# Kernel optimization log

Measured on AMD Instinct MI355X. Metric: run time of the kernel, lower is better.

Reference implementation:

```python
import jax, jax.numpy as jnp
import numpy as np

CLASS_NUM = 31
KERNEL_NUM = 5
KERNEL_MUL = 2.0


def setup_inputs() -> dict:
    key = jax.random.key(0)
    k1, k2, k3, k4 = jax.random.split(key, 4)
    B, D = 4096, 256
    source = jax.random.normal(k1, (B, D), dtype=jnp.float32)
    target = jax.random.normal(k2, (B, D), dtype=jnp.float32)
    s_label = jax.random.randint(k3, (B,), 0, CLASS_NUM, dtype=jnp.int64)
    t_label = jax.random.uniform(k4, (B, CLASS_NUM), dtype=jnp.float32)
    return {"source": source, "target": target, "s_label": s_label, "t_label": t_label}


def _cal_weight(s_label, t_label):
    # Source: one-hot, column-normalized (empty classes -> divide by 100)
    s_onehot = jax.nn.one_hot(s_label, CLASS_NUM, dtype=jnp.float32)
    s_cnt = jnp.sum(s_onehot, axis=0)
    s_vec = s_onehot / jnp.where(s_cnt == 0, 100.0, s_cnt)
    # Target: soft probs, column-normalized (detached in original)
    t_prob = jax.lax.stop_gradient(t_label)
    t_cnt = jnp.sum(t_prob, axis=0)
    t_vec = t_prob / jnp.where(t_cnt == 0, 100.0, t_cnt)
    # Classes present in BOTH source labels and target argmax predictions
    t_arg = jnp.argmax(t_prob, axis=1)
    t_present = jnp.sum(jax.nn.one_hot(t_arg, CLASS_NUM, dtype=jnp.float32), axis=0) > 0
    mask = ((s_cnt > 0) & t_present).astype(jnp.float32)
    n_idx = jnp.maximum(jnp.sum(mask), 1.0)
    s_vec = s_vec * mask
    t_vec = t_vec * mask
    w_ss = (s_vec @ s_vec.T) / n_idx
    w_tt = (t_vec @ t_vec.T) / n_idx
    w_st = (s_vec @ t_vec.T) / n_idx
    return w_ss, w_tt, w_st


def reference(source, target, s_label, t_label):
    B = source.shape[0]
    w_ss, w_tt, w_st = _cal_weight(s_label, t_label)

    # Multi-bandwidth RBF kernel over concatenated samples
    total = jnp.concatenate([source, target], axis=0)  # [2B, D]
    sq = jnp.sum(total * total, axis=1)
    l2 = jnp.maximum(sq[:, None] + sq[None, :] - 2.0 * (total @ total.T), 0.0)  # [2B, 2B]

    n = 2 * B
    bw = jnp.sum(jax.lax.stop_gradient(l2)) / float(max(n * n - n, 1))
    bw = jnp.maximum(bw, 1e-6) / (KERNEL_MUL ** (KERNEL_NUM // 2))
    kernels = jnp.zeros_like(l2)
    for i in range(KERNEL_NUM):
        kernels = kernels + jnp.exp(-l2 / jnp.maximum(bw * KERNEL_MUL ** i, 1e-6))

    ss = kernels[:B, :B]
    tt = kernels[B:, B:]
    st = kernels[:B, B:]
    loss = jnp.sum(w_ss * ss + w_tt * tt - 2.0 * w_st * st)
    return loss
```

## Files before the change

### kernel.cpp

```cpp
#include <hip/hip_runtime.h>
#include <cstddef>


#define B 4096
#define D 256
#define C 31
#define N2 8192
#define NTILE 64
#define NBLK (NTILE * (NTILE + 1) / 2)

typedef __attribute__((ext_vector_type(8))) short bf16x8;
typedef __attribute__((ext_vector_type(4))) float f32x4;

struct WS {
  float inv_n_idx;
  float inv_d4;
  float pSumsq[256];
  unsigned pTpres[128];
  alignas(16) float pMsum[256 * 256];
  alignas(16) int pScnt[128 * 32];
  alignas(16) float pTcnt[128 * 32];
  float sq[N2];
  int slab[N2];
  float sdv[N2];
  alignas(16) unsigned char Thi8[(size_t)N2 * D];
  alignas(16) unsigned short vhi[(size_t)N2 * 32];
  alignas(16) double part[NBLK];
};

static __device__ __forceinline__ unsigned short f2bf(float f) {
  unsigned int u = __float_as_uint(f);
  return (unsigned short)((u + 0x7fffu + ((u >> 16) & 1u)) >> 16);
}
static __device__ __forceinline__ float bf2f(unsigned short s) {
  return __uint_as_float(((unsigned int)s) << 16);
}
static __device__ __forceinline__ float exp2_hw(float x) {
  float r;
  asm("v_exp_f32 %0, %1" : "=v"(r) : "v"(x));
  return r;
}

#define GLD16(gsrc, ldst)                                                     \
  __builtin_amdgcn_global_load_lds(                                           \
      (const __attribute__((address_space(1))) void*)(gsrc),                  \
      (__attribute__((address_space(3))) void*)(ldst), 16, 0, 0)

__global__ __launch_bounds__(256) void kPrep(const float* __restrict__ src,
                                             const float* __restrict__ tgt,
                                             const int* __restrict__ s_label,
                                             const float* __restrict__ t_label,
                                             WS* __restrict__ ws) {
  int tid = threadIdx.x, w = tid >> 6, lane = tid & 63;
  int blk = blockIdx.x;
  int r0 = blk * 32;
  bool is_src = (r0 < B);
  __shared__ float rsq[32];
  __shared__ float colp[4][256];
  __shared__ int ls[32];
  __shared__ float lt[8][32];
  __shared__ int lpres[32];
  if (tid < 32) { ls[tid] = 0; lpres[tid] = 0; }

  const float* basep =
      is_src ? src + (size_t)r0 * D : tgt + (size_t)(r0 - B) * D;

  float4 xv[8];
#pragma unroll
  for (int i = 0; i < 8; ++i)
    xv[i] = *(const float4*)(basep + (size_t)(w * 8 + i) * D + lane * 4);

  float ca0 = 0.f, ca1 = 0.f, ca2 = 0.f, ca3 = 0.f;
  int sc = lane >> 4, gl = (lane >> 1) & 7, hf = lane & 1;
#pragma unroll
  for (int i = 0; i < 8; ++i) {
    int rr = w * 8 + i;
    int p = r0 + rr;
    float4 x = xv[i];
    unsigned int pk = __builtin_amdgcn_cvt_pk_fp8_f32(x.x, x.y, 0, false);
    pk = __builtin_amdgcn_cvt_pk_fp8_f32(x.z, x.w, pk, true);
    int gp = (gl + p + (p >> 1)) & 7;
    *(unsigned int*)(&ws->Thi8[(size_t)p * D + sc * 64 + gp * 8 + hf * 4]) = pk;
    ca0 += x.x; ca1 += x.y; ca2 += x.z; ca3 += x.w;
    float s = x.x * x.x + x.y * x.y + x.z * x.z + x.w * x.w;
#pragma unroll
    for (int off = 32; off; off >>= 1) s += __shfl_down(s, off, 64);
    if (lane == 0) rsq[rr] = s;
  }
  colp[w][lane * 4 + 0] = ca0;
  colp[w][lane * 4 + 1] = ca1;
  colp[w][lane * 4 + 2] = ca2;
  colp[w][lane * 4 + 3] = ca3;

  if (!is_src) {
    int g = tid >> 5, c = tid & 31;
    float s = 0.f;
    if (c < C) {
#pragma unroll
      for (int k = 0; k < 4; ++k)
        s += t_label[(size_t)(r0 - B + g * 4 + k) * C + c];
    }
    lt[g][c] = s;
    int rr = tid >> 3, j = tid & 7;
    float best = -1e30f;
    int barg = 0;
    for (int c2 = j; c2 < C; c2 += 8) {
      float x = t_label[(size_t)(r0 - B + rr) * C + c2];
      if (x > best) { best = x; barg = c2; }
    }
#pragma unroll
    for (int m = 1; m < 8; m <<= 1) {
      float ob = __shfl_xor(best, m, 64);
      int oa = __shfl_xor(barg, m, 64);
      if (ob > best || (ob == best && oa < barg)) { best = ob; barg = oa; }
    }
    if (j == 0) lpres[barg] = 1;
  }
  __syncthreads();

  if (tid < 32) {
    int p = r0 + tid;
    ws->sq[p] = rsq[tid];
    if (is_src) {
      int lb = s_label[p];
      ws->slab[p] = lb;
      atomicAdd(&ls[lb], 1);
    } else {
      ws->slab[p] = 0;
    }
  }
  if (tid < 64) {
    float ss = (tid < 32) ? rsq[tid] : 0.f;
#pragma unroll
    for (int off = 32; off; off >>= 1) ss += __shfl_down(ss, off, 64);
    if (tid == 0) ws->pSumsq[blk] = ss;
  }
  ws->pMsum[blk * 256 + tid] =
      colp[0][tid] + colp[1][tid] + colp[2][tid] + colp[3][tid];
  __syncthreads();
  if (is_src) {
    if (tid < 32) ws->pScnt[blk * 32 + tid] = ls[tid];
  } else {
    if (tid < 32) {
      float s = 0.f;
#pragma unroll
      for (int g = 0; g < 8; ++g) s += lt[g][tid];
      ws->pTcnt[(blk - 128) * 32 + tid] = s;
    }
    if (tid < 64) {
      int bit = (tid < 32) ? lpres[tid] : 0;
      unsigned long long bal = __ballot(bit != 0);
      if (tid == 0) ws->pTpres[blk - 128] = (unsigned)bal;
    }
  }
}

__global__ __launch_bounds__(256) void kFin(const float* __restrict__ t_label,
                                            WS* __restrict__ ws) {
  int tid = threadIdx.x, w = tid >> 6, lane = tid & 63;
  __shared__ float sdiv[32], tdiv[32];
  __shared__ int rs[8][32];
  __shared__ float rt[8][32];
  __shared__ unsigned pm[2];
  __shared__ double dm[4], dsq[4];

  {
    int g = tid >> 5, c = tid & 31;
    int cs = 0;
    float ts = 0.f;
#pragma unroll
    for (int k = 0; k < 16; ++k) {
      cs += ws->pScnt[(g * 16 + k) * 32 + c];
      ts += ws->pTcnt[(g * 16 + k) * 32 + c];
    }
    rs[g][c] = cs;
    rt[g][c] = ts;
  }
  if (tid < 128) {
    unsigned m = ws->pTpres[tid];
#pragma unroll
    for (int off = 32; off; off >>= 1) m |= __shfl_down(m, off, 64);
    if ((tid & 63) == 0) pm[tid >> 6] = m;
  }
  __syncthreads();

  if (tid < 64) {
    int m = 0;
    if (tid < 32) {
      int cnt = 0;
      float t = 0.f;
#pragma unroll
      for (int g = 0; g < 8; ++g) { cnt += rs[g][tid]; t += rt[g][tid]; }
      unsigned pres = pm[0] | pm[1];
      m = (tid < C) && (cnt > 0) && ((pres >> tid) & 1u);
      sdiv[tid] = m ? 1.f / (float)cnt : 0.f;
      tdiv[tid] = m ? 1.f / ((t == 0.f) ? 100.f : t) : 0.f;
    }
    unsigned long long bal = __ballot(m);
    if (tid == 0 && blockIdx.x == 0)
      ws->inv_n_idx = 1.f / fmaxf((float)__popcll(bal), 1.f);
  }

  if (blockIdx.x == 0) {
    double m = 0.0;
    for (int b2 = 0; b2 < 256; ++b2) m += (double)ws->pMsum[b2 * 256 + tid];
    double msq = m * m;
    double ssq = (double)ws->pSumsq[tid];
#pragma unroll
    for (int off = 32; off; off >>= 1) {
      msq += __shfl_down(msq, off, 64);
      ssq += __shfl_down(ssq, off, 64);
    }
    if (lane == 0) { dm[w] = msq; dsq[w] = ssq; }
    __syncthreads();
    if (tid == 0) {
      double MSQ = dm[0] + dm[1] + dm[2] + dm[3];
      double S = dsq[0] + dsq[1] + dsq[2] + dsq[3];
      double n = (double)N2;
      double sum_l2 = 2.0 * n * S - 2.0 * MSQ;
      double bw = sum_l2 / (n * n - n);
      bw = fmax(bw, 1e-6) * 0.25;
      ws->inv_d4 = (float)(1.0 / fmax(bw * 16.0, 1e-6));
    }
  }
  __syncthreads();

  int p = blockIdx.x * 256 + tid;
  if (p < B) {
    ws->sdv[p] = sdiv[ws->slab[p]];
  } else {
    ws->sdv[p] = 0.f;
    const float* r = t_label + (size_t)(p - B) * C;
    float vrow[32];
#pragma unroll
    for (int c = 0; c < 32; ++c) vrow[c] = (c < C) ? -r[c] * tdiv[c] : 0.f;
#pragma unroll
    for (int k = 0; k < 8; ++k) {
      ushort4 vh;
      vh.x = f2bf(vrow[k * 4 + 0]);
      vh.y = f2bf(vrow[k * 4 + 1]);
      vh.z = f2bf(vrow[k * 4 + 2]);
      vh.w = f2bf(vrow[k * 4 + 3]);
      *(ushort4*)(&ws->vhi[(size_t)p * 32 + k * 4]) = vh;
    }
  }
}

template <int KIND, bool DIAG>
static __device__ __forceinline__ float epi_ss_st(
    const f32x4 (&acc)[4][4], float ci2, const float* tSq, const int* tSlab,
    const float* tSdv, const unsigned short* Vsw, int p0, int q0, int wr,
    int wc, int mrow, int quad) {
  float k2 = 2.f * ci2;
  float cq[4], sdq[4];
  int lq[4];
#pragma unroll
  for (int tj = 0; tj < 4; ++tj) {
    int iq = 128 + wc + tj * 16 + mrow;
    cq[tj] = -ci2 * tSq[iq];
    if (KIND == 0) {
      lq[tj] = tSlab[iq];
      sdq[tj] = tSdv[iq];
    }
  }
  float local = 0.f;
#pragma unroll
  for (int ti = 0; ti < 4; ++ti) {
#pragma unroll
    for (int rg = 0; rg < 4; ++rg) {
      int ip = wr + ti * 16 + quad * 4 + rg;
      float cpl = -ci2 * tSq[ip];
      int lp = tSlab[ip];
      float sp = tSdv[ip];
#pragma unroll
      for (int tj = 0; tj < 4; ++tj) {
        float z = fminf(fmaf(k2, acc[ti][tj][rg], cpl + cq[tj]), 0.f);
        float y = exp2_hw(z);
        float kv = y;
        y *= y; kv += y;
        y *= y; kv += y;
        y *= y; kv += y;
        y *= y; kv += y;
        float wv;
        if (KIND == 0) {
          wv = (lp == lq[tj]) ? sp * sdq[tj] : 0.f;
        } else {
          int ql = wc + tj * 16 + mrow;
          wv = sp * bf2f(Vsw[ql * 32 + ((lp + ql) & 31)]);
        }
        if (DIAG) {
          int p = p0 + ip;
          int q = q0 + wc + tj * 16 + mrow;
          float f = (q > p) ? 2.f : ((q == p) ? 1.f : 0.f);
          local = fmaf(wv * f, kv, local);
        } else {
          local = fmaf(wv, kv, local);
        }
      }
    }
  }
  if (!DIAG) local *= 2.f;
  return local;
}

template <bool DIAG>
static __device__ __forceinline__ float epi_tt(const f32x4 (&acc)[4][4],
                                               float ci2, const float* tSq,
                                               const unsigned short* SA,
                                               const unsigned short* SB,
                                               int p0, int q0, int wr, int wc,
                                               int mrow, int quad) {
  float k2 = 2.f * ci2;
  float cq[4];
#pragma unroll
  for (int tj = 0; tj < 4; ++tj)
    cq[tj] = -ci2 * tSq[128 + wc + tj * 16 + mrow];
  float cp[16];
#pragma unroll
  for (int ti = 0; ti < 4; ++ti)
#pragma unroll
    for (int rg = 0; rg < 4; ++rg)
      cp[ti * 4 + rg] = -ci2 * tSq[wr + ti * 16 + quad * 4 + rg];
  bf16x8 af[4], bfr[4];
#pragma unroll
  for (int ti = 0; ti < 4; ++ti)
    af[ti] = *(const bf16x8*)(SA + (wr + ti * 16 + mrow) * 32 + quad * 8);
#pragma unroll
  for (int tj = 0; tj < 4; ++tj)
    bfr[tj] = *(const bf16x8*)(SB + (wc + tj * 16 + mrow) * 32 + quad * 8);
  float local = 0.f;
#pragma unroll
  for (int ti = 0; ti < 4; ++ti) {
#pragma unroll
    for (int tj = 0; tj < 4; ++tj) {
      f32x4 wv4 = __builtin_amdgcn_mfma_f32_16x16x32_bf16(
          af[ti], bfr[tj], (f32x4){0.f, 0.f, 0.f, 0.f}, 0, 0, 0);
#pragma unroll
      for (int rg = 0; rg < 4; ++rg) {
        float z = fminf(fmaf(k2, acc[ti][tj][rg], cp[ti * 4 + rg] + cq[tj]), 0.f);
        float y = exp2_hw(z);
        float kv = y;
        y *= y; kv += y;
        y *= y; kv += y;
        y *= y; kv += y;
        y *= y; kv += y;
        if (DIAG) {
          int p = p0 + wr + ti * 16 + quad * 4 + rg;
          int q = q0 + wc + tj * 16 + mrow;
          float f = (q > p) ? 2.f : ((q == p) ? 1.f : 0.f);
          local = fmaf(wv4[rg] * f, kv, local);
        } else {
          local = fmaf(wv4[rg], kv, local);
        }
      }
    }
  }
  if (!DIAG) local *= 2.f;
  return local;
}

static __device__ __forceinline__ void do_chunk(const unsigned char* fb,
                                                f32x4 (&acc)[4][4],
                                                const int (&aAdr)[4],
                                                const int (&bAdr)[4]) {
#pragma unroll
  for (int t = 0; t < 2; ++t) {
    const int x = t << 5;
    long aF[4], bF[4];
#pragma unroll
    for (int ti = 0; ti < 4; ++ti)
      aF[ti] = *(const long*)(fb + (aAdr[ti] ^ x));
#pragma unroll
    for (int tj = 0; tj < 4; ++tj)
      bF[tj] = *(const long*)(fb + 8192 + (bAdr[tj] ^ x));
#pragma unroll
    for (int ti = 0; ti < 4; ++ti)
#pragma unroll
      for (int tj = 0; tj < 4; ++tj)
        acc[ti][tj] = __builtin_amdgcn_mfma_f32_16x16x32_fp8_fp8(
            aF[ti], bF[tj], acc[ti][tj], 0, 0, 0);
  }
}

#define WBAR(N)                                                               \
  do {                                                                        \
    asm volatile("s_waitcnt vmcnt(" #N ")" ::: "memory");                     \
    __builtin_amdgcn_s_barrier();                                             \
    asm volatile("" ::: "memory");                                            \
  } while (0)

__global__ __launch_bounds__(256, 3) void k3_main(WS* __restrict__ ws) {
  int tid = threadIdx.x, w = tid >> 6, lane = tid & 63;
  int lin0 = blockIdx.x;
  int e = (lin0 & 7) * (NBLK / 8) + (lin0 >> 3);
  int b = 0, nb = 484, rem = e;
  while (rem >= nb) { rem -= nb; ++b; nb -= 64; }
  int base = b * 8;
  int bq_, r;
  if (rem < 36) {
    bq_ = 0;
    while ((bq_ + 1) * (bq_ + 2) / 2 <= rem) ++bq_;
    r = rem - (bq_ * (bq_ + 1)) / 2;
  } else {
    int t = rem - 36;
    bq_ = 8 + (t >> 3);
    r = t & 7;
  }
  int bp = base + r, bq = base + bq_;
  int p0 = bp * 128, q0 = bq * 128;

  bool is_ss = (bq < 32);
  bool is_tt = (bp >= 32);
  bool is_st = !is_ss && !is_tt;

  __shared__ __align__(16) unsigned char S[3][2][8192];
  __shared__ __align__(16) float tSq[256];
  __shared__ __align__(16) int tSlab[256];
  __shared__ __align__(16) float tSdv[256];
  unsigned short* Vsw = (unsigned short*)&S[1][0][0];
  unsigned short* SA = (unsigned short*)&S[1][0][0];
  unsigned short* SB = (unsigned short*)&S[1][1][0];
  double* red = (double*)&S[2][0][0];

  const int wr = (w >> 1) * 64, wc = (w & 1) * 64;
  const int mrow = lane & 15, quad = lane >> 4;
  f32x4 acc[4][4];
#pragma unroll
  for (int i = 0; i < 4; ++i)
#pragma unroll
    for (int j = 0; j < 4; ++j) acc[i][j] = (f32x4){0.f, 0.f, 0.f, 0.f};

  const unsigned char* T8 = ws->Thi8;
  int rA = tid >> 2, cb16 = (tid & 3) * 16, cp8 = (tid & 3) * 8;
  const unsigned char* a_lo = T8 + (size_t)(p0 + rA) * D + cb16;
  const unsigned char* a_hi = a_lo + (size_t)64 * D;
  const unsigned char* b_lo = T8 + (size_t)(q0 + rA) * D + cb16;
  const unsigned char* b_hi = b_lo + (size_t)64 * D;

#define STAGE(bufi, off)                                                      \
  do {                                                                        \
    GLD16(a_lo + (off), &S[bufi][0][w * 1024]);                               \
    GLD16(a_hi + (off), &S[bufi][0][w * 1024 + 4096]);                        \
    GLD16(b_lo + (off), &S[bufi][1][w * 1024]);                               \
    GLD16(b_hi + (off), &S[bufi][1][w * 1024 + 4096]);                        \
  } while (0)

  int aAdr[4], bAdr[4];
#pragma unroll
  for (int ti = 0; ti < 4; ++ti) {
    int Ra = wr + ti * 16 + mrow;
    aAdr[ti] = Ra * 64 + (((quad + Ra + (Ra >> 1)) & 7) << 3);
    int Rb = wc + ti * 16 + mrow;
    bAdr[ti] = Rb * 64 + (((quad + Rb + (Rb >> 1)) & 7) << 3);
  }

  uint4 stv0 = {0, 0, 0, 0}, stv1 = {0, 0, 0, 0};

  STAGE(0, 0);
  STAGE(1, 64);
  {
    int l32 = lane & 31;
    const float* s1 = ((lane < 32) ? ws->sq + p0 : ws->sq + q0) + l32 * 4;
    GLD16(s1, tSq);
    const int* s2 = ((lane < 32) ? ws->slab + p0 : ws->slab + q0) + l32 * 4;
    GLD16(s2, tSlab);
    const float* s3 = ((lane < 32) ? ws->sdv + p0 : ws->sdv + q0) + l32 * 4;
    GLD16(s3, tSdv);
  }
  WBAR(7);

  STAGE(2, 128);
  do_chunk(&S[0][0][0], acc, aAdr, bAdr);
  WBAR(7);

  STAGE(0, 192);
  do_chunk(&S[1][0][0], acc, aAdr, bAdr);
  WBAR(4);

  if (is_st) {
    const uint4* vsrc = (const uint4*)(ws->vhi + (size_t)(q0 + (tid >> 1)) * 32 +
                                       (tid & 1) * 16);
    stv0 = vsrc[0];
    stv1 = vsrc[1];
  }
  do_chunk(&S[2][0][0], acc, aAdr, bAdr);
  if (is_st) {
    WBAR(2);
  } else {
    WBAR(0);
  }

  if (is_tt) {
    const unsigned short* gA = ws->vhi + (size_t)(p0 + rA) * 32 + cp8;
    const unsigned short* gB = ws->vhi + (size_t)(q0 + rA) * 32 + cp8;
    GLD16(gA, &S[1][0][w * 1024]);
    GLD16(gA + (size_t)64 * 32, &S[1][0][w * 1024 + 4096]);
    GLD16(gB, &S[1][1][w * 1024]);
    GLD16(gB + (size_t)64 * 32, &S[1][1][w * 1024 + 4096]);
  }
  do_chunk(&S[0][0][0], acc, aAdr, bAdr);

  if (is_st) {
    int rr = tid >> 1, h = (tid & 1) * 16;
    unsigned int uu[8] = {stv0.x, stv0.y, stv0.z, stv0.w,
                          stv1.x, stv1.y, stv1.z, stv1.w};
#pragma unroll
    for (int j = 0; j < 8; ++j) {
      Vsw[rr * 32 + ((h + 2 * j + rr) & 31)] = (unsigned short)(uu[j] & 0xffff);
      Vsw[rr * 32 + ((h + 2 * j + 1 + rr) & 31)] = (unsigned short)(uu[j] >> 16);
    }
  }
  __syncthreads();

  float ci2 = ws->inv_d4 * 1.44269504f;
  float local;
  if (is_ss) {
    if (bp == bq)
      local = epi_ss_st<0, true>(acc, ci2, tSq, tSlab, tSdv, Vsw, p0, q0, wr,
                                 wc, mrow, quad);
    else
      local = epi_ss_st<0, false>(acc, ci2, tSq, tSlab, tSdv, Vsw, p0, q0, wr,
                                  wc, mrow, quad);
  } else if (is_st) {
    local = epi_ss_st<1, false>(acc, ci2, tSq, tSlab, tSdv, Vsw, p0, q0, wr,
                                wc, mrow, quad);
  } else {
    if (bp == bq)
      local = epi_tt<true>(acc, ci2, tSq, SA, SB, p0, q0, wr, wc, mrow, quad);
    else
      local = epi_tt<false>(acc, ci2, tSq, SA, SB, p0, q0, wr, wc, mrow, quad);
  }

  double dl = (double)local;
#pragma unroll
  for (int off = 32; off; off >>= 1) dl += __shfl_down(dl, off, 64);
  if (lane == 0) red[w] = dl;
  __syncthreads();
  if (tid == 0) ws->part[lin0] = red[0] + red[1] + red[2] + red[3];
#undef STAGE
}

__global__ __launch_bounds__(256) void k4_out(WS* __restrict__ ws,
                                              float* __restrict__ out) {
  __shared__ double sh[4];
  int tid = threadIdx.x, w = tid >> 6, lane = tid & 63;
  double s = 0.0;
  for (int i = tid; i < NBLK; i += 256) s += ws->part[i];
#pragma unroll
  for (int off = 32; off; off >>= 1) s += __shfl_down(s, off, 64);
  if (lane == 0) sh[w] = s;
  __syncthreads();
  if (tid == 0)
    out[0] = (float)((sh[0] + sh[1] + sh[2] + sh[3]) * (double)ws->inv_n_idx);
}

extern "C" void kernel_launch(void* const* d_in, const int* in_sizes, int n_in,
                              void* d_out, int out_size, void* d_ws, size_t ws_size,
                              hipStream_t stream) {
  const float* src = (const float*)d_in[0];
  const float* tgt = (const float*)d_in[1];
  const int* s_label = (const int*)d_in[2];
  const float* t_label = (const float*)d_in[3];
  float* out = (float*)d_out;
  WS* ws = (WS*)d_ws;

  kPrep<<<256, 256, 0, stream>>>(src, tgt, s_label, t_label, ws);
  kFin<<<32, 256, 0, stream>>>(t_label, ws);
  k3_main<<<NBLK, 256, 0, stream>>>(ws);
  k4_out<<<1, 256, 0, stream>>>(ws, out);
}
```

Baseline: 112.1 us.

## Repack FP8 tile layout for 16-byte LDS fragment loads and halve prep rows

```diff
diff --git a/kernel.cpp b/kernel.cpp
--- a/kernel.cpp
+++ b/kernel.cpp
@@ -11,15 +11,16 @@
 
 typedef __attribute__((ext_vector_type(8))) short bf16x8;
 typedef __attribute__((ext_vector_type(4))) float f32x4;
+typedef __attribute__((ext_vector_type(2))) long lx2;
 
 struct WS {
   float inv_n_idx;
   float inv_d4;
-  float pSumsq[256];
-  unsigned pTpres[128];
-  alignas(16) float pMsum[256 * 256];
-  alignas(16) int pScnt[128 * 32];
-  alignas(16) float pTcnt[128 * 32];
+  float pSumsq[512];
+  unsigned pTpres[256];
+  alignas(16) float pMsum[512 * 256];
+  alignas(16) int pScnt[256 * 32];
+  alignas(16) float pTcnt[256 * 32];
   float sq[N2];
   int slab[N2];
   float sdv[N2];
@@ -53,9 +54,9 @@
                                              WS* __restrict__ ws) {
   int tid = threadIdx.x, w = tid >> 6, lane = tid & 63;
   int blk = blockIdx.x;
-  int r0 = blk * 32;
-  bool is_src = (r0 < B);
-  __shared__ float rsq[32];
+  int r0 = blk * 16;
+  bool is_src = (blk < 256);
+  __shared__ float rsq[16];
   __shared__ float colp[4][256];
   __shared__ int ls[32];
   __shared__ float lt[8][32];
@@ -65,26 +66,26 @@
   const float* basep =
       is_src ? src + (size_t)r0 * D : tgt + (size_t)(r0 - B) * D;
 
-  float4 xv[8];
-#pragma unroll
-  for (int i = 0; i < 8; ++i)
-    xv[i] = *(const float4*)(basep + (size_t)(w * 8 + i) * D + lane * 4);
+  float4 xv[4];
+#pragma unroll
+  for (int i = 0; i < 4; ++i)
+    xv[i] = *(const float4*)(basep + (size_t)(w * 4 + i) * D + lane * 4);
 
   float ca0 = 0.f, ca1 = 0.f, ca2 = 0.f, ca3 = 0.f;
   int sc = lane >> 4, gl = (lane >> 1) & 7, hf = lane & 1;
 #pragma unroll
-  for (int i = 0; i < 8; ++i) {
-    int rr = w * 8 + i;
+  for (int i = 0; i < 4; ++i) {
+    int rr = w * 4 + i;
     int p = r0 + rr;
     float4 x = xv[i];
     unsigned int pk = __builtin_amdgcn_cvt_pk_fp8_f32(x.x, x.y, 0, false);
     pk = __builtin_amdgcn_cvt_pk_fp8_f32(x.z, x.w, pk, true);
-    int gp = (gl + p + (p >> 1)) & 7;
-    *(unsigned int*)(&ws->Thi8[(size_t)p * D + sc * 64 + gp * 8 + hf * 4]) = pk;
+    int off = ((((gl & 3) + (p >> 1)) & 3) << 4) + ((gl >> 2) << 3) + hf * 4;
+    *(unsigned int*)(&ws->Thi8[(size_t)p * D + sc * 64 + off]) = pk;
     ca0 += x.x; ca1 += x.y; ca2 += x.z; ca3 += x.w;
     float s = x.x * x.x + x.y * x.y + x.z * x.z + x.w * x.w;
 #pragma unroll
-    for (int off = 32; off; off >>= 1) s += __shfl_down(s, off, 64);
+    for (int off2 = 32; off2; off2 >>= 1) s += __shfl_down(s, off2, 64);
     if (lane == 0) rsq[rr] = s;
   }
   colp[w][lane * 4 + 0] = ca0;
@@ -97,19 +98,19 @@
     float s = 0.f;
     if (c < C) {
 #pragma unroll
-      for (int k = 0; k < 4; ++k)
-        s += t_label[(size_t)(r0 - B + g * 4 + k) * C + c];
+      for (int k = 0; k < 2; ++k)
+        s += t_label[(size_t)(r0 - B + g * 2 + k) * C + c];
     }
     lt[g][c] = s;
-    int rr = tid >> 3, j = tid & 7;
+    int rr = tid >> 4, j = tid & 15;
     float best = -1e30f;
     int barg = 0;
-    for (int c2 = j; c2 < C; c2 += 8) {
+    for (int c2 = j; c2 < C; c2 += 16) {
       float x = t_label[(size_t)(r0 - B + rr) * C + c2];
       if (x > best) { best = x; barg = c2; }
     }
 #pragma unroll
-    for (int m = 1; m < 8; m <<= 1) {
+    for (int m = 1; m < 16; m <<= 1) {
       float ob = __shfl_xor(best, m, 64);
       int oa = __shfl_xor(barg, m, 64);
       if (ob > best || (ob == best && oa < barg)) { best = ob; barg = oa; }
@@ -118,7 +119,7 @@
   }
   __syncthreads();
 
-  if (tid < 32) {
+  if (tid < 16) {
     int p = r0 + tid;
     ws->sq[p] = rsq[tid];
     if (is_src) {
@@ -130,9 +131,9 @@
     }
   }
   if (tid < 64) {
-    float ss = (tid < 32) ? rsq[tid] : 0.f;
-#pragma unroll
-    for (int off = 32; off; off >>= 1) ss += __shfl_down(ss, off, 64);
+    float ss = (tid < 16) ? rsq[tid] : 0.f;
+#pragma unroll
+    for (int off2 = 32; off2; off2 >>= 1) ss += __shfl_down(ss, off2, 64);
     if (tid == 0) ws->pSumsq[blk] = ss;
   }
   ws->pMsum[blk * 256 + tid] =
@@ -145,12 +146,12 @@
       float s = 0.f;
 #pragma unroll
       for (int g = 0; g < 8; ++g) s += lt[g][tid];
-      ws->pTcnt[(blk - 128) * 32 + tid] = s;
+      ws->pTcnt[(blk - 256) * 32 + tid] = s;
     }
     if (tid < 64) {
       int bit = (tid < 32) ? lpres[tid] : 0;
       unsigned long long bal = __ballot(bit != 0);
-      if (tid == 0) ws->pTpres[blk - 128] = (unsigned)bal;
+      if (tid == 0) ws->pTpres[blk - 256] = (unsigned)bal;
     }
   }
 }
@@ -161,7 +162,7 @@
   __shared__ float sdiv[32], tdiv[32];
   __shared__ int rs[8][32];
   __shared__ float rt[8][32];
-  __shared__ unsigned pm[2];
+  __shared__ unsigned pm[4];
   __shared__ double dm[4], dsq[4];
 
   {
@@ -169,18 +170,18 @@
     int cs = 0;
     float ts = 0.f;
 #pragma unroll
-    for (int k = 0; k < 16; ++k) {
-      cs += ws->pScnt[(g * 16 + k) * 32 + c];
-      ts += ws->pTcnt[(g * 16 + k) * 32 + c];
+    for (int k = 0; k < 32; ++k) {
+      cs += ws->pScnt[(g * 32 + k) * 32 + c];
+      ts += ws->pTcnt[(g * 32 + k) * 32 + c];
     }
     rs[g][c] = cs;
     rt[g][c] = ts;
   }
-  if (tid < 128) {
+  {
     unsigned m = ws->pTpres[tid];
 #pragma unroll
     for (int off = 32; off; off >>= 1) m |= __shfl_down(m, off, 64);
-    if ((tid & 63) == 0) pm[tid >> 6] = m;
+    if (lane == 0) pm[w] = m;
   }
   __syncthreads();
 
@@ -191,7 +192,7 @@
       float t = 0.f;
 #pragma unroll
       for (int g = 0; g < 8; ++g) { cnt += rs[g][tid]; t += rt[g][tid]; }
-      unsigned pres = pm[0] | pm[1];
+      unsigned pres = pm[0] | pm[1] | pm[2] | pm[3];
       m = (tid < C) && (cnt > 0) && ((pres >> tid) & 1u);
       sdiv[tid] = m ? 1.f / (float)cnt : 0.f;
       tdiv[tid] = m ? 1.f / ((t == 0.f) ? 100.f : t) : 0.f;
@@ -203,9 +204,9 @@
 
   if (blockIdx.x == 0) {
     double m = 0.0;
-    for (int b2 = 0; b2 < 256; ++b2) m += (double)ws->pMsum[b2 * 256 + tid];
+    for (int b2 = 0; b2 < 512; ++b2) m += (double)ws->pMsum[b2 * 256 + tid];
     double msq = m * m;
-    double ssq = (double)ws->pSumsq[tid];
+    double ssq = (double)(ws->pSumsq[tid] + ws->pSumsq[256 + tid]);
 #pragma unroll
     for (int off = 32; off; off >>= 1) {
       msq += __shfl_down(msq, off, 64);
@@ -363,23 +364,19 @@
                                                 f32x4 (&acc)[4][4],
                                                 const int (&aAdr)[4],
                                                 const int (&bAdr)[4]) {
-#pragma unroll
-  for (int t = 0; t < 2; ++t) {
-    const int x = t << 5;
-    long aF[4], bF[4];
-#pragma unroll
-    for (int ti = 0; ti < 4; ++ti)
-      aF[ti] = *(const long*)(fb + (aAdr[ti] ^ x));
-#pragma unroll
-    for (int tj = 0; tj < 4; ++tj)
-      bF[tj] = *(const long*)(fb + 8192 + (bAdr[tj] ^ x));
+  lx2 aF[4], bF[4];
+#pragma unroll
+  for (int ti = 0; ti < 4; ++ti) aF[ti] = *(const lx2*)(fb + aAdr[ti]);
+#pragma unroll
+  for (int tj = 0; tj < 4; ++tj) bF[tj] = *(const lx2*)(fb + 8192 + bAdr[tj]);
+#pragma unroll
+  for (int t = 0; t < 2; ++t)
 #pragma unroll
     for (int ti = 0; ti < 4; ++ti)
 #pragma unroll
       for (int tj = 0; tj < 4; ++tj)
         acc[ti][tj] = __builtin_amdgcn_mfma_f32_16x16x32_fp8_fp8(
-            aF[ti], bF[tj], acc[ti][tj], 0, 0, 0);
-  }
+            aF[ti][t], bF[tj][t], acc[ti][tj], 0, 0, 0);
 }
 
 #define WBAR(N)                                                               \
@@ -449,9 +446,9 @@
 #pragma unroll
   for (int ti = 0; ti < 4; ++ti) {
     int Ra = wr + ti * 16 + mrow;
-    aAdr[ti] = Ra * 64 + (((quad + Ra + (Ra >> 1)) & 7) << 3);
+    aAdr[ti] = Ra * 64 + (((quad + (Ra >> 1)) & 3) << 4);
     int Rb = wc + ti * 16 + mrow;
-    bAdr[ti] = Rb * 64 + (((quad + Rb + (Rb >> 1)) & 7) << 3);
+    bAdr[ti] = Rb * 64 + (((quad + (Rb >> 1)) & 3) << 4);
   }
 
   uint4 stv0 = {0, 0, 0, 0}, stv1 = {0, 0, 0, 0};
@@ -564,7 +561,7 @@
   float* out = (float*)d_out;
   WS* ws = (WS*)d_ws;
 
-  kPrep<<<256, 256, 0, stream>>>(src, tgt, s_label, t_label, ws);
+  kPrep<<<512, 256, 0, stream>>>(src, tgt, s_label, t_label, ws);
   kFin<<<32, 256, 0, stream>>>(t_label, ws);
   k3_main<<<NBLK, 256, 0, stream>>>(ws);
   k4_out<<<1, 256, 0, stream>>>(ws, out);
```

Result: slower. 125.2 us (+11.6%).
